# Kernel optimization log

Measured on AMD Instinct MI355X. Metric: run time of the kernel, lower is better.

Reference implementation:

```python
import jax, jax.numpy as jnp
import numpy as np

N, CIN, H, W = 8, 128, 56, 56
COUT, KH, KW = 128, 3, 3
STRIDE, PAD, DIL = 1, 1, 1
HO = (H + 2 * PAD - DIL * (KH - 1) - 1) // STRIDE + 1
WO = (W + 2 * PAD - DIL * (KW - 1) - 1) // STRIDE + 1
K = KH * KW


def setup_inputs() -> dict:
    key = jax.random.key(0)
    k1, k2, k3, k4, k5 = jax.random.split(key, 5)
    x = jax.random.normal(k1, (N, CIN, H, W), dtype=jnp.float32)
    offset = jax.random.normal(k2, (N, 2 * K, HO, WO), dtype=jnp.float32)
    weight = jax.random.normal(k3, (COUT, CIN, KH, KW), dtype=jnp.float32) * (1.0 / np.sqrt(CIN * K))
    bias = jax.random.normal(k4, (COUT,), dtype=jnp.float32) * 0.01
    x2 = jax.random.normal(k5, (N, COUT, HO, WO), dtype=jnp.float32)
    return {"x": x, "offset": offset, "weight": weight, "bias": bias, "x2": x2}


def _deform_conv2d(x, offset, weight, bias):
    n, c, h, w = x.shape
    cout = weight.shape[0]
    # offset layout (torchvision): channels = [dy_0, dx_0, dy_1, dx_1, ...]
    off = offset.reshape(n, K, 2, HO, WO)
    ki = jnp.arange(KH).repeat(KW)          # kernel row index per k   [K]
    kj = jnp.tile(jnp.arange(KW), KH)       # kernel col index per k   [K]
    base_y = (jnp.arange(HO) * STRIDE - PAD)[None, :, None] + (ki * DIL)[:, None, None]  # [K,HO,1]
    base_x = (jnp.arange(WO) * STRIDE - PAD)[None, None, :] + (kj * DIL)[:, None, None]  # [K,1,WO]
    py = base_y[None].astype(x.dtype) + off[:, :, 0]   # [N,K,HO,WO]
    px = base_x[None].astype(x.dtype) + off[:, :, 1]   # [N,K,HO,WO]

    y0 = jnp.floor(py).astype(jnp.int32)
    x0 = jnp.floor(px).astype(jnp.int32)
    wy = py - y0.astype(x.dtype)
    wx = px - x0.astype(x.dtype)

    xf = x.reshape(n, c, h * w)

    def gather(yi, xi):
        valid = (yi >= 0) & (yi < h) & (xi >= 0) & (xi < w)        # [N,K,HO,WO]
        lin = jnp.clip(yi, 0, h - 1) * w + jnp.clip(xi, 0, w - 1)  # [N,K,HO,WO]
        v = jax.vmap(lambda xfn, idx: xfn[:, idx])(xf, lin)        # [N,C,K,HO,WO]
        return v * valid[:, None].astype(x.dtype)

    v00 = gather(y0, x0)
    v01 = gather(y0, x0 + 1)
    v10 = gather(y0 + 1, x0)
    v11 = gather(y0 + 1, x0 + 1)
    wy = wy[:, None]
    wx = wx[:, None]
    cols = (v00 * (1 - wy) * (1 - wx) + v01 * (1 - wy) * wx
            + v10 * wy * (1 - wx) + v11 * wy * wx)                 # [N,C,K,HO,WO]

    wmat = weight.reshape(cout, c, K)
    out = jnp.einsum('nckhw,ock->nohw', cols, wmat)
    return out + bias[None, :, None, None]


def reference(x, offset, weight, bias, x2):
    out = _deform_conv2d(x, offset, weight, bias)
    return jax.nn.relu(out + x2)
```

## Files before the change

### kernel.cpp

```cpp
#include <hip/hip_runtime.h>

#define N_IMG 8
#define CIN   128
#define H_IN  56
#define W_IN  56
#define COUT  128
#define HW    3136
#define TROWS 9
#define TILE_B (TROWS * 56 * 256)
#define PLA_OFF TILE_B
#define PLW_OFF (PLA_OFF + 18432)
#define PLC_OFF (PLW_OFF + 9216)
#define SMEM_TOTAL (PLC_OFF + 4608)

typedef __attribute__((ext_vector_type(8))) short short8;
typedef __attribute__((ext_vector_type(4))) float f32x4;
typedef _Float16 h8 __attribute__((ext_vector_type(8)));

__device__ __forceinline__ unsigned short hb(float f) {
    _Float16 h = (_Float16)f;
    return __builtin_bit_cast(unsigned short, h);
}
__device__ __forceinline__ h8 splat8(unsigned short b) {
    _Float16 s = __builtin_bit_cast(_Float16, b);
    return (h8){s, s, s, s, s, s, s, s};
}
__device__ __forceinline__ void gload16(const void* g, void* l) {
    __builtin_amdgcn_global_load_lds(
        (const __attribute__((address_space(1))) unsigned int*)g,
        (__attribute__((address_space(3))) unsigned int*)l, 16, 0, 0);
}

__global__ __launch_bounds__(256) void prep_kernel(const float* __restrict__ x,
                                                   const float* __restrict__ w,
                                                   unsigned short* __restrict__ xt,
                                                   unsigned short* __restrict__ wr) {
    int b = blockIdx.x;
    int tid = threadIdx.x;
    if (b < 784) {
        int c = tid & 127;
        int half = tid >> 7;
        int n = b / 98;
        int hw0 = (b - n * 98) * 32 + half * 16;
        const float* xp = x + ((size_t)(n * CIN + c)) * HW + hw0;
        unsigned short* op = xt + ((size_t)n * HW + hw0) * CIN + c;
#pragma unroll
        for (int r = 0; r < 16; ++r) op[r * CIN] = hb(xp[r]);
    } else {
        int G = (b - 784) * 256 + tid;
        int lane = G & 63;
        int f = (G >> 6) & 7;
        int kc4 = (G >> 9) & 3;
        int tap = G >> 11;
        int cout = f * 16 + (lane & 15);
        int ch = kc4 * 32 + (lane >> 4) * 8;
        short8 v;
#pragma unroll
        for (int j = 0; j < 8; ++j)
            v[j] = (short)hb(w[((size_t)cout * CIN + ch + j) * 9 + tap]);
        *(short8*)(wr + (size_t)G * 8) = v;
    }
}

__global__ __launch_bounds__(512, 2) void deform_main(
    const float* __restrict__ offset, const float* __restrict__ x2,
    const float* __restrict__ bias, const unsigned short* __restrict__ xt,
    const unsigned short* __restrict__ wr, float* __restrict__ out)
{
    extern __shared__ char smem[];
    int4*  plA = (int4*)(smem + PLA_OFF);
    uint2* plW = (uint2*)(smem + PLW_OFF);
    int*   plC = (int*)(smem + PLC_OFF);

    int tid = threadIdx.x;
    int orig = blockIdx.x;
    int n   = orig & 7;
    int ro0 = (orig >> 3) * 2;

    const char* xim = (const char*)(xt + (size_t)n * HW * CIN);

#pragma unroll
    for (int s = 0; s < 16; ++s) {
        int d = s * 8192 + tid * 16;
        if (d < TILE_B) {
            int p = d >> 8;
            int tr = p / 56;
            int tx = p - tr * 56;
            int gy = min(max(ro0 - 3 + tr, 0), 55);
            int c  = ((d >> 4) & 15) ^ (p & 15);
            gload16(xim + (((gy * 56 + tx) << 8) + (c << 4)), smem + d);
        }
    }

    for (int e = tid; e < 1152; e += 512) {
        int r = (e >= 576) ? 1 : 0;
        int e2 = e - r * 576;
        int tap = e2 >> 6;
        int px  = e2 & 63;
        int wo  = min(px, 55);
        int hor = ro0 + r;
        const float* offp = offset + ((size_t)n * 18 + tap * 2) * HW + hor * 56 + wo;
        float offy = offp[0];
        float offx = offp[HW];
        int ki = tap / 3;
        int kj = tap - ki * 3;
        float py  = (float)(hor - 1 + ki) + offy;
        float pxf = (float)(wo - 1 + kj) + offx;
        float y0f = floorf(py), x0f = floorf(pxf);
        float wy = py - y0f, wx = pxf - x0f;
        int y0 = (int)y0f, x0 = (int)x0f;
        int y1 = y0 + 1, x1 = x0 + 1;
        bool vy0 = (y0 >= 0) && (y0 < H_IN);
        bool vy1 = (y1 >= 0) && (y1 < H_IN);
        bool vx0 = (x0 >= 0) && (x0 < W_IN);
        bool vx1 = (x1 >= 0) && (x1 < W_IN);
        int cy0 = min(max(y0, 0), 55), cy1 = min(max(y1, 0), 55);
        int cx0 = min(max(x0, 0), 55), cx1 = min(max(x1, 0), 55);
        float w00 = (vy0 && vx0) ? (1.f - wy) * (1.f - wx) : 0.f;
        float w01 = (vy0 && vx1) ? (1.f - wy) * wx : 0.f;
        float w10 = (vy1 && vx0) ? wy * (1.f - wx) : 0.f;
        float w11 = (vy1 && vx1) ? wy * wx : 0.f;
        int f0 = (y0 < ro0 - 3 || y0 > ro0 + 5) ? 1 : 0;
        int f1 = (y1 < ro0 - 3 || y1 > ro0 + 5) ? 1 : 0;
        int tr0 = min(max(cy0 + 3 - ro0, 0), TROWS - 1);
        int tr1 = min(max(cy1 + 3 - ro0, 0), TROWS - 1);
        int p00 = tr0 * 56 + cx0, p01 = tr0 * 56 + cx1;
        int p10 = tr1 * 56 + cx0, p11 = tr1 * 56 + cx1;
        int4 A;
        A.x = ((p00 << 8) | ((p00 & 15) << 4)) | ((f0 && w00 != 0.f) ? 0x80000000 : 0);
        A.y = ((p01 << 8) | ((p01 & 15) << 4)) | ((f0 && w01 != 0.f) ? 0x80000000 : 0);
        A.z = ((p10 << 8) | ((p10 & 15) << 4)) | ((f1 && w10 != 0.f) ? 0x80000000 : 0);
        A.w = ((p11 << 8) | ((p11 & 15) << 4)) | ((f1 && w11 != 0.f) ? 0x80000000 : 0);
        plA[e] = A;
        uint2 W;
        W.x = (unsigned)hb(w00) | ((unsigned)hb(w01) << 16);
        W.y = (unsigned)hb(w10) | ((unsigned)hb(w11) << 16);
        plW[e] = W;
        plC[e] = cy0 | (cy1 << 6) | (cx0 << 12) | (cx1 << 18);
    }
    __syncthreads();

    int lane = tid & 63;
    int w8 = tid >> 6;
    int kg = w8 & 1;
    int mt = w8 >> 1;
    int llo = lane & 15, lhi = lane >> 4;
    int slot0 = mt * 32 + llo;
    int slot1 = slot0 + 16;
    int eb0 = (slot0 >> 6) * 576 + (slot0 & 63);
    int eb1 = (slot1 >> 6) * 576 + (slot1 & 63);
    const char* wrb = (const char*)wr;
    int cbs0 = ((kg * 2 + 0) * 4 + lhi) << 4;
    int cbs1 = ((kg * 2 + 1) * 4 + lhi) << 4;

    f32x4 acc[2][8] = {};

    int4  A0 = plA[eb0], A1 = plA[eb1];
    uint2 W0 = plW[eb0], W1 = plW[eb1];

    for (int tap = 0; tap < 9; ++tap) {
        int4 nA0, nA1; uint2 nW0, nW1;
        if (tap < 8) {
            nA0 = plA[eb0 + (tap + 1) * 64]; nW0 = plW[eb0 + (tap + 1) * 64];
            nA1 = plA[eb1 + (tap + 1) * 64]; nW1 = plW[eb1 + (tap + 1) * 64];
        }
        bool fa0 = (unsigned)A0.x >> 31, fa1 = (unsigned)A0.y >> 31;
        bool fa2 = (unsigned)A0.z >> 31, fa3 = (unsigned)A0.w >> 31;
        bool fc0 = (unsigned)A1.x >> 31, fc1 = (unsigned)A1.y >> 31;
        bool fc2 = (unsigned)A1.z >> 31, fc3 = (unsigned)A1.w >> 31;
        bool anyfb = __any(fa0 | fa1 | fa2 | fa3 | fc0 | fc1 | fc2 | fc3);
        int gpa0 = 0, gpa1 = 0, gpa2 = 0, gpa3 = 0;
        int gpc0 = 0, gpc1 = 0, gpc2 = 0, gpc3 = 0;
        if (anyfb) {
            int C0 = plC[eb0 + tap * 64];
            int C1 = plC[eb1 + tap * 64];
            gpa0 = ((C0 & 63) * 56 + ((C0 >> 12) & 63)) << 8;
            gpa1 = ((C0 & 63) * 56 + ((C0 >> 18) & 63)) << 8;
            gpa2 = (((C0 >> 6) & 63) * 56 + ((C0 >> 12) & 63)) << 8;
            gpa3 = (((C0 >> 6) & 63) * 56 + ((C0 >> 18) & 63)) << 8;
            gpc0 = ((C1 & 63) * 56 + ((C1 >> 12) & 63)) << 8;
            gpc1 = ((C1 & 63) * 56 + ((C1 >> 18) & 63)) << 8;
            gpc2 = (((C1 >> 6) & 63) * 56 + ((C1 >> 12) & 63)) << 8;
            gpc3 = (((C1 >> 6) & 63) * 56 + ((C1 >> 18) & 63)) << 8;
        }

#pragma unroll
        for (int kc = 0; kc < 2; ++kc) {
            int cbs = kc ? cbs1 : cbs0;
            const char* bb = wrb + (size_t)((tap * 4 + kg * 2 + kc) * 8) * 1024 + lane * 16;
            h8 bf[8];
#pragma unroll
            for (int f = 0; f < 8; ++f)
                bf[f] = *(const h8*)(bb + f * 1024);

            h8 g0 = *(const h8*)(smem + ((A0.x & 0x7FFFFFFF) ^ cbs));
            h8 g1 = *(const h8*)(smem + ((A0.y & 0x7FFFFFFF) ^ cbs));
            h8 g2 = *(const h8*)(smem + ((A0.z & 0x7FFFFFFF) ^ cbs));
            h8 g3 = *(const h8*)(smem + ((A0.w & 0x7FFFFFFF) ^ cbs));
            if (anyfb) {
                if (fa0) g0 = *(const h8*)(xim + (size_t)(gpa0 + cbs));
                if (fa1) g1 = *(const h8*)(xim + (size_t)(gpa1 + cbs));
                if (fa2) g2 = *(const h8*)(xim + (size_t)(gpa2 + cbs));
                if (fa3) g3 = *(const h8*)(xim + (size_t)(gpa3 + cbs));
            }
            h8 a0 = g0 * splat8((unsigned short)(W0.x & 0xFFFF))
                  + g1 * splat8((unsigned short)(W0.x >> 16))
                  + g2 * splat8((unsigned short)(W0.y & 0xFFFF))
                  + g3 * splat8((unsigned short)(W0.y >> 16));

            h8 h0 = *(const h8*)(smem + ((A1.x & 0x7FFFFFFF) ^ cbs));
            h8 h1 = *(const h8*)(smem + ((A1.y & 0x7FFFFFFF) ^ cbs));
            h8 h2 = *(const h8*)(smem + ((A1.z & 0x7FFFFFFF) ^ cbs));
            h8 h3 = *(const h8*)(smem + ((A1.w & 0x7FFFFFFF) ^ cbs));
            if (anyfb) {
                if (fc0) h0 = *(const h8*)(xim + (size_t)(gpc0 + cbs));
                if (fc1) h1 = *(const h8*)(xim + (size_t)(gpc1 + cbs));
                if (fc2) h2 = *(const h8*)(xim + (size_t)(gpc2 + cbs));
                if (fc3) h3 = *(const h8*)(xim + (size_t)(gpc3 + cbs));
            }
            h8 a1 = h0 * splat8((unsigned short)(W1.x & 0xFFFF))
                  + h1 * splat8((unsigned short)(W1.x >> 16))
                  + h2 * splat8((unsigned short)(W1.y & 0xFFFF))
                  + h3 * splat8((unsigned short)(W1.y >> 16));

#pragma unroll
            for (int f = 0; f < 8; ++f) {
                acc[0][f] = __builtin_amdgcn_mfma_f32_16x16x32_f16(a0, bf[f], acc[0][f], 0, 0, 0);
                acc[1][f] = __builtin_amdgcn_mfma_f32_16x16x32_f16(a1, bf[f], acc[1][f], 0, 0, 0);
            }
        }
        A0 = nA0; A1 = nA1; W0 = nW0; W1 = nW1;
    }

    __syncthreads();
    if (kg == 1) {
#pragma unroll
        for (int q = 0; q < 2; ++q)
#pragma unroll
            for (int f = 0; f < 8; ++f)
                *(f32x4*)(smem + ((((mt * 2 + q) * 8 + f) << 10) + (lane << 4))) = acc[q][f];
    }
    __syncthreads();
    if (kg == 0) {
#pragma unroll
        for (int q = 0; q < 2; ++q)
#pragma unroll
            for (int f = 0; f < 8; ++f) {
                size_t ro = (((mt * 2 + q) * 8 + f) << 10) + (lane << 4);
                acc[q][f] += *(const f32x4*)(smem + ro);
            }

#pragma unroll
        for (int q = 0; q < 2; ++q) {
            int slotq = mt * 32 + q * 16 + lhi * 4;
            int srow = slotq >> 6;
            int wo4 = slotq & 63;
            if (wo4 < 56) {
#pragma unroll
                for (int f = 0; f < 8; ++f) {
                    int cout = f * 16 + llo;
                    float bb = bias[cout];
                    size_t off = ((size_t)(n * COUT + cout)) * HW + (ro0 + srow) * 56 + wo4;
                    f32x4 xv = *(const f32x4*)(x2 + off);
                    f32x4 o;
#pragma unroll
                    for (int r = 0; r < 4; ++r) {
                        float v = acc[q][f][r] + bb + xv[r];
                        o[r] = v > 0.f ? v : 0.f;
                    }
                    *(f32x4*)(out + off) = o;
                }
            }
        }
    }
}

extern "C" void kernel_launch(void* const* d_in, const int* in_sizes, int n_in,
                              void* d_out, int out_size, void* d_ws, size_t ws_size,
                              hipStream_t stream) {
    const float* x      = (const float*)d_in[0];
    const float* offset = (const float*)d_in[1];
    const float* weight = (const float*)d_in[2];
    const float* bias   = (const float*)d_in[3];
    const float* x2     = (const float*)d_in[4];
    float* out = (float*)d_out;

    unsigned short* xt = (unsigned short*)d_ws;
    unsigned short* wr = (unsigned short*)((char*)d_ws + 6422528ULL);

    hipFuncSetAttribute((const void*)deform_main,
                        hipFuncAttributeMaxDynamicSharedMemorySize, SMEM_TOTAL);
    prep_kernel<<<856, 256, 0, stream>>>(x, weight, xt, wr);
    deform_main<<<224, 512, SMEM_TOTAL, stream>>>(offset, x2, bias, xt, wr, out);
}
```

Measured before the change: 32.31 us.

## Software-pipeline LDS gathers one k-chunk ahead of MFMA compute in deform conv

Restructures the tap loop into a double-buffered pipeline. The bilinear corner gathers (LDS reads plus the rare global fallback) for the next k-chunk are issued before the MFMAs of the current chunk, using two register sets. This is meant to hide LDS and global gather latency behind matrix-core work. The cost is higher VGPR pressure, which could lower occupancy or cause spills.

```diff
diff --git a/kernel.cpp b/kernel.cpp
--- a/kernel.cpp
+++ b/kernel.cpp
@@ -30,6 +30,69 @@
         (const __attribute__((address_space(1))) unsigned int*)g,
         (__attribute__((address_space(3))) unsigned int*)l, 16, 0, 0);
 }
+
+#define ISSUE(TAPV, CBS, PA0, PA1, G0,G1,G2,G3,H0,H1,H2,H3)                    \
+  {                                                                            \
+    G0 = *(const h8*)(smem + ((PA0.x & 0x7FFFFFFF) ^ (CBS)));                  \
+    G1 = *(const h8*)(smem + ((PA0.y & 0x7FFFFFFF) ^ (CBS)));                  \
+    G2 = *(const h8*)(smem + ((PA0.z & 0x7FFFFFFF) ^ (CBS)));                  \
+    G3 = *(const h8*)(smem + ((PA0.w & 0x7FFFFFFF) ^ (CBS)));                  \
+    H0 = *(const h8*)(smem + ((PA1.x & 0x7FFFFFFF) ^ (CBS)));                  \
+    H1 = *(const h8*)(smem + ((PA1.y & 0x7FFFFFFF) ^ (CBS)));                  \
+    H2 = *(const h8*)(smem + ((PA1.z & 0x7FFFFFFF) ^ (CBS)));                  \
+    H3 = *(const h8*)(smem + ((PA1.w & 0x7FFFFFFF) ^ (CBS)));                  \
+    bool qa0 = (unsigned)PA0.x >> 31, qa1 = (unsigned)PA0.y >> 31;             \
+    bool qa2 = (unsigned)PA0.z >> 31, qa3 = (unsigned)PA0.w >> 31;             \
+    bool qc0 = (unsigned)PA1.x >> 31, qc1 = (unsigned)PA1.y >> 31;             \
+    bool qc2 = (unsigned)PA1.z >> 31, qc3 = (unsigned)PA1.w >> 31;             \
+    if (__any(qa0 | qa1 | qa2 | qa3 | qc0 | qc1 | qc2 | qc3)) {                \
+      int C0 = plC[eb0 + (TAPV) * 64], C1 = plC[eb1 + (TAPV) * 64];            \
+      if (qa0) G0 = *(const h8*)(xim + (size_t)(int)((((C0 & 63) * 56 + ((C0 >> 12) & 63)) << 8) + (CBS))); \
+      if (qa1) G1 = *(const h8*)(xim + (size_t)(int)((((C0 & 63) * 56 + ((C0 >> 18) & 63)) << 8) + (CBS))); \
+      if (qa2) G2 = *(const h8*)(xim + (size_t)(int)(((((C0 >> 6) & 63) * 56 + ((C0 >> 12) & 63)) << 8) + (CBS))); \
+      if (qa3) G3 = *(const h8*)(xim + (size_t)(int)(((((C0 >> 6) & 63) * 56 + ((C0 >> 18) & 63)) << 8) + (CBS))); \
+      if (qc0) H0 = *(const h8*)(xim + (size_t)(int)((((C1 & 63) * 56 + ((C1 >> 12) & 63)) << 8) + (CBS))); \
+      if (qc1) H1 = *(const h8*)(xim + (size_t)(int)((((C1 & 63) * 56 + ((C1 >> 18) & 63)) << 8) + (CBS))); \
+      if (qc2) H2 = *(const h8*)(xim + (size_t)(int)(((((C1 >> 6) & 63) * 56 + ((C1 >> 12) & 63)) << 8) + (CBS))); \
+      if (qc3) H3 = *(const h8*)(xim + (size_t)(int)(((((C1 >> 6) & 63) * 56 + ((C1 >> 18) & 63)) << 8) + (CBS))); \
+    }                                                                          \
+  }
+
+#define COMPUTE(G0,G1,G2,G3,H0,H1,H2,H3, PW0, PW1, BB)                         \
+  {                                                                            \
+    h8 b0 = *(const h8*)((BB));                                                \
+    h8 b1 = *(const h8*)((BB) + 1024);                                         \
+    h8 b2 = *(const h8*)((BB) + 2048);                                         \
+    h8 b3 = *(const h8*)((BB) + 3072);                                         \
+    h8 b4 = *(const h8*)((BB) + 4096);                                         \
+    h8 b5 = *(const h8*)((BB) + 5120);                                         \
+    h8 b6 = *(const h8*)((BB) + 6144);                                         \
+    h8 b7 = *(const h8*)((BB) + 7168);                                         \
+    h8 a0 = G0 * splat8((unsigned short)(PW0.x & 0xFFFF))                      \
+          + G1 * splat8((unsigned short)(PW0.x >> 16))                         \
+          + G2 * splat8((unsigned short)(PW0.y & 0xFFFF))                      \
+          + G3 * splat8((unsigned short)(PW0.y >> 16));                        \
+    h8 a1 = H0 * splat8((unsigned short)(PW1.x & 0xFFFF))                      \
+          + H1 * splat8((unsigned short)(PW1.x >> 16))                         \
+          + H2 * splat8((unsigned short)(PW1.y & 0xFFFF))                      \
+          + H3 * splat8((unsigned short)(PW1.y >> 16));                        \
+    acc[0][0] = __builtin_amdgcn_mfma_f32_16x16x32_f16(a0, b0, acc[0][0], 0, 0, 0); \
+    acc[1][0] = __builtin_amdgcn_mfma_f32_16x16x32_f16(a1, b0, acc[1][0], 0, 0, 0); \
+    acc[0][1] = __builtin_amdgcn_mfma_f32_16x16x32_f16(a0, b1, acc[0][1], 0, 0, 0); \
+    acc[1][1] = __builtin_amdgcn_mfma_f32_16x16x32_f16(a1, b1, acc[1][1], 0, 0, 0); \
+    acc[0][2] = __builtin_amdgcn_mfma_f32_16x16x32_f16(a0, b2, acc[0][2], 0, 0, 0); \
+    acc[1][2] = __builtin_amdgcn_mfma_f32_16x16x32_f16(a1, b2, acc[1][2], 0, 0, 0); \
+    acc[0][3] = __builtin_amdgcn_mfma_f32_16x16x32_f16(a0, b3, acc[0][3], 0, 0, 0); \
+    acc[1][3] = __builtin_amdgcn_mfma_f32_16x16x32_f16(a1, b3, acc[1][3], 0, 0, 0); \
+    acc[0][4] = __builtin_amdgcn_mfma_f32_16x16x32_f16(a0, b4, acc[0][4], 0, 0, 0); \
+    acc[1][4] = __builtin_amdgcn_mfma_f32_16x16x32_f16(a1, b4, acc[1][4], 0, 0, 0); \
+    acc[0][5] = __builtin_amdgcn_mfma_f32_16x16x32_f16(a0, b5, acc[0][5], 0, 0, 0); \
+    acc[1][5] = __builtin_amdgcn_mfma_f32_16x16x32_f16(a1, b5, acc[1][5], 0, 0, 0); \
+    acc[0][6] = __builtin_amdgcn_mfma_f32_16x16x32_f16(a0, b6, acc[0][6], 0, 0, 0); \
+    acc[1][6] = __builtin_amdgcn_mfma_f32_16x16x32_f16(a1, b6, acc[1][6], 0, 0, 0); \
+    acc[0][7] = __builtin_amdgcn_mfma_f32_16x16x32_f16(a0, b7, acc[0][7], 0, 0, 0); \
+    acc[1][7] = __builtin_amdgcn_mfma_f32_16x16x32_f16(a1, b7, acc[1][7], 0, 0, 0); \
+  }
 
 __global__ __launch_bounds__(256) void prep_kernel(const float* __restrict__ x,
                                                    const float* __restrict__ w,
@@ -158,78 +221,28 @@
     int4  A0 = plA[eb0], A1 = plA[eb1];
     uint2 W0 = plW[eb0], W1 = plW[eb1];
 
-    for (int tap = 0; tap < 9; ++tap) {
+    h8 xa0, xa1, xa2, xa3, ya0, ya1, ya2, ya3;
+    h8 xb0, xb1, xb2, xb3, yb0, yb1, yb2, yb3;
+    ISSUE(0, cbs0, A0, A1, xa0, xa1, xa2, xa3, ya0, ya1, ya2, ya3);
+
+    for (int t = 0; t < 9; ++t) {
         int4 nA0, nA1; uint2 nW0, nW1;
-        if (tap < 8) {
-            nA0 = plA[eb0 + (tap + 1) * 64]; nW0 = plW[eb0 + (tap + 1) * 64];
-            nA1 = plA[eb1 + (tap + 1) * 64]; nW1 = plW[eb1 + (tap + 1) * 64];
-        }
-        bool fa0 = (unsigned)A0.x >> 31, fa1 = (unsigned)A0.y >> 31;
-        bool fa2 = (unsigned)A0.z >> 31, fa3 = (unsigned)A0.w >> 31;
-        bool fc0 = (unsigned)A1.x >> 31, fc1 = (unsigned)A1.y >> 31;
-        bool fc2 = (unsigned)A1.z >> 31, fc3 = (unsigned)A1.w >> 31;
-        bool anyfb = __any(fa0 | fa1 | fa2 | fa3 | fc0 | fc1 | fc2 | fc3);
-        int gpa0 = 0, gpa1 = 0, gpa2 = 0, gpa3 = 0;
-        int gpc0 = 0, gpc1 = 0, gpc2 = 0, gpc3 = 0;
-        if (anyfb) {
-            int C0 = plC[eb0 + tap * 64];
-            int C1 = plC[eb1 + tap * 64];
-            gpa0 = ((C0 & 63) * 56 + ((C0 >> 12) & 63)) << 8;
-            gpa1 = ((C0 & 63) * 56 + ((C0 >> 18) & 63)) << 8;
-            gpa2 = (((C0 >> 6) & 63) * 56 + ((C0 >> 12) & 63)) << 8;
-            gpa3 = (((C0 >> 6) & 63) * 56 + ((C0 >> 18) & 63)) << 8;
-            gpc0 = ((C1 & 63) * 56 + ((C1 >> 12) & 63)) << 8;
-            gpc1 = ((C1 & 63) * 56 + ((C1 >> 18) & 63)) << 8;
-            gpc2 = (((C1 >> 6) & 63) * 56 + ((C1 >> 12) & 63)) << 8;
-            gpc3 = (((C1 >> 6) & 63) * 56 + ((C1 >> 18) & 63)) << 8;
-        }
-
-#pragma unroll
-        for (int kc = 0; kc < 2; ++kc) {
-            int cbs = kc ? cbs1 : cbs0;
-            const char* bb = wrb + (size_t)((tap * 4 + kg * 2 + kc) * 8) * 1024 + lane * 16;
-            h8 bf[8];
-#pragma unroll
-            for (int f = 0; f < 8; ++f)
-                bf[f] = *(const h8*)(bb + f * 1024);
-
-            h8 g0 = *(const h8*)(smem + ((A0.x & 0x7FFFFFFF) ^ cbs));
-            h8 g1 = *(const h8*)(smem + ((A0.y & 0x7FFFFFFF) ^ cbs));
-            h8 g2 = *(const h8*)(smem + ((A0.z & 0x7FFFFFFF) ^ cbs));
-            h8 g3 = *(const h8*)(smem + ((A0.w & 0x7FFFFFFF) ^ cbs));
-            if (anyfb) {
-                if (fa0) g0 = *(const h8*)(xim + (size_t)(gpa0 + cbs));
-                if (fa1) g1 = *(const h8*)(xim + (size_t)(gpa1 + cbs));
-                if (fa2) g2 = *(const h8*)(xim + (size_t)(gpa2 + cbs));
-                if (fa3) g3 = *(const h8*)(xim + (size_t)(gpa3 + cbs));
-            }
-            h8 a0 = g0 * splat8((unsigned short)(W0.x & 0xFFFF))
-                  + g1 * splat8((unsigned short)(W0.x >> 16))
-                  + g2 * splat8((unsigned short)(W0.y & 0xFFFF))
-                  + g3 * splat8((unsigned short)(W0.y >> 16));
-
-            h8 h0 = *(const h8*)(smem + ((A1.x & 0x7FFFFFFF) ^ cbs));
-            h8 h1 = *(const h8*)(smem + ((A1.y & 0x7FFFFFFF) ^ cbs));
-            h8 h2 = *(const h8*)(smem + ((A1.z & 0x7FFFFFFF) ^ cbs));
-            h8 h3 = *(const h8*)(smem + ((A1.w & 0x7FFFFFFF) ^ cbs));
-            if (anyfb) {
-                if (fc0) h0 = *(const h8*)(xim + (size_t)(gpc0 + cbs));
-                if (fc1) h1 = *(const h8*)(xim + (size_t)(gpc1 + cbs));
-                if (fc2) h2 = *(const h8*)(xim + (size_t)(gpc2 + cbs));
-                if (fc3) h3 = *(const h8*)(xim + (size_t)(gpc3 + cbs));
-            }
-            h8 a1 = h0 * splat8((unsigned short)(W1.x & 0xFFFF))
-                  + h1 * splat8((unsigned short)(W1.x >> 16))
-                  + h2 * splat8((unsigned short)(W1.y & 0xFFFF))
-                  + h3 * splat8((unsigned short)(W1.y >> 16));
-
-#pragma unroll
-            for (int f = 0; f < 8; ++f) {
-                acc[0][f] = __builtin_amdgcn_mfma_f32_16x16x32_f16(a0, bf[f], acc[0][f], 0, 0, 0);
-                acc[1][f] = __builtin_amdgcn_mfma_f32_16x16x32_f16(a1, bf[f], acc[1][f], 0, 0, 0);
-            }
-        }
-        A0 = nA0; A1 = nA1; W0 = nW0; W1 = nW1;
+        if (t < 8) {
+            nA0 = plA[eb0 + (t + 1) * 64]; nA1 = plA[eb1 + (t + 1) * 64];
+            nW0 = plW[eb0 + (t + 1) * 64]; nW1 = plW[eb1 + (t + 1) * 64];
+        }
+        ISSUE(t, cbs1, A0, A1, xb0, xb1, xb2, xb3, yb0, yb1, yb2, yb3);
+        {
+            const char* bb = wrb + (size_t)((t * 4 + kg * 2 + 0) * 8) * 1024 + lane * 16;
+            COMPUTE(xa0, xa1, xa2, xa3, ya0, ya1, ya2, ya3, W0, W1, bb);
+        }
+        if (t < 8)
+            ISSUE(t + 1, cbs0, nA0, nA1, xa0, xa1, xa2, xa3, ya0, ya1, ya2, ya3);
+        {
+            const char* bb = wrb + (size_t)((t * 4 + kg * 2 + 1) * 8) * 1024 + lane * 16;
+            COMPUTE(xb0, xb1, xb2, xb3, yb0, yb1, yb2, yb3, W0, W1, bb);
+        }
+        if (t < 8) { A0 = nA0; A1 = nA1; W0 = nW0; W1 = nW1; }
     }
 
     __syncthreads();
```

Result: slower. 37.12 us (+14.9%).

## Route half the sampling slots through global memory gathers instead of LDS

Applied to the files above, without the earlier changes.

Pixel slots whose bit 4 is set now get plain global-image byte offsets in the prepass, with no tile-relative LDS address or fallback flag. In the main loop the second slot group (A1) always gathers from global memory, issued early in each kc iteration, while the first group still reads from LDS with the fallback path. The MFMA loops are split so the a0 products can run while the global loads for a1 are in flight. This is meant to relieve LDS bandwidth pressure by spreading gathers across LDS and L1/L2, at the cost of higher-latency global loads. It also assumes every slot1 (A1) pixel has bit 4 set in the prepass, which depends on the slot-to-pixel mapping and is not visible here.

```diff
diff --git a/kernel.cpp b/kernel.cpp
--- a/kernel.cpp
+++ b/kernel.cpp
@@ -120,17 +120,24 @@
         float w01 = (vy0 && vx1) ? (1.f - wy) * wx : 0.f;
         float w10 = (vy1 && vx0) ? wy * (1.f - wx) : 0.f;
         float w11 = (vy1 && vx1) ? wy * wx : 0.f;
-        int f0 = (y0 < ro0 - 3 || y0 > ro0 + 5) ? 1 : 0;
-        int f1 = (y1 < ro0 - 3 || y1 > ro0 + 5) ? 1 : 0;
-        int tr0 = min(max(cy0 + 3 - ro0, 0), TROWS - 1);
-        int tr1 = min(max(cy1 + 3 - ro0, 0), TROWS - 1);
-        int p00 = tr0 * 56 + cx0, p01 = tr0 * 56 + cx1;
-        int p10 = tr1 * 56 + cx0, p11 = tr1 * 56 + cx1;
         int4 A;
-        A.x = ((p00 << 8) | ((p00 & 15) << 4)) | ((f0 && w00 != 0.f) ? 0x80000000 : 0);
-        A.y = ((p01 << 8) | ((p01 & 15) << 4)) | ((f0 && w01 != 0.f) ? 0x80000000 : 0);
-        A.z = ((p10 << 8) | ((p10 & 15) << 4)) | ((f1 && w10 != 0.f) ? 0x80000000 : 0);
-        A.w = ((p11 << 8) | ((p11 & 15) << 4)) | ((f1 && w11 != 0.f) ? 0x80000000 : 0);
+        if ((px >> 4) & 1) {
+            A.x = (cy0 * 56 + cx0) << 8;
+            A.y = (cy0 * 56 + cx1) << 8;
+            A.z = (cy1 * 56 + cx0) << 8;
+            A.w = (cy1 * 56 + cx1) << 8;
+        } else {
+            int f0 = (y0 < ro0 - 3 || y0 > ro0 + 5) ? 1 : 0;
+            int f1 = (y1 < ro0 - 3 || y1 > ro0 + 5) ? 1 : 0;
+            int tr0 = min(max(cy0 + 3 - ro0, 0), TROWS - 1);
+            int tr1 = min(max(cy1 + 3 - ro0, 0), TROWS - 1);
+            int p00 = tr0 * 56 + cx0, p01 = tr0 * 56 + cx1;
+            int p10 = tr1 * 56 + cx0, p11 = tr1 * 56 + cx1;
+            A.x = ((p00 << 8) | ((p00 & 15) << 4)) | ((f0 && w00 != 0.f) ? 0x80000000 : 0);
+            A.y = ((p01 << 8) | ((p01 & 15) << 4)) | ((f0 && w01 != 0.f) ? 0x80000000 : 0);
+            A.z = ((p10 << 8) | ((p10 & 15) << 4)) | ((f1 && w10 != 0.f) ? 0x80000000 : 0);
+            A.w = ((p11 << 8) | ((p11 & 15) << 4)) | ((f1 && w11 != 0.f) ? 0x80000000 : 0);
+        }
         plA[e] = A;
         uint2 W;
         W.x = (unsigned)hb(w00) | ((unsigned)hb(w01) << 16);
@@ -166,27 +173,23 @@
         }
         bool fa0 = (unsigned)A0.x >> 31, fa1 = (unsigned)A0.y >> 31;
         bool fa2 = (unsigned)A0.z >> 31, fa3 = (unsigned)A0.w >> 31;
-        bool fc0 = (unsigned)A1.x >> 31, fc1 = (unsigned)A1.y >> 31;
-        bool fc2 = (unsigned)A1.z >> 31, fc3 = (unsigned)A1.w >> 31;
-        bool anyfb = __any(fa0 | fa1 | fa2 | fa3 | fc0 | fc1 | fc2 | fc3);
+        bool anyfb = __any(fa0 | fa1 | fa2 | fa3);
         int gpa0 = 0, gpa1 = 0, gpa2 = 0, gpa3 = 0;
-        int gpc0 = 0, gpc1 = 0, gpc2 = 0, gpc3 = 0;
         if (anyfb) {
             int C0 = plC[eb0 + tap * 64];
-            int C1 = plC[eb1 + tap * 64];
             gpa0 = ((C0 & 63) * 56 + ((C0 >> 12) & 63)) << 8;
             gpa1 = ((C0 & 63) * 56 + ((C0 >> 18) & 63)) << 8;
             gpa2 = (((C0 >> 6) & 63) * 56 + ((C0 >> 12) & 63)) << 8;
             gpa3 = (((C0 >> 6) & 63) * 56 + ((C0 >> 18) & 63)) << 8;
-            gpc0 = ((C1 & 63) * 56 + ((C1 >> 12) & 63)) << 8;
-            gpc1 = ((C1 & 63) * 56 + ((C1 >> 18) & 63)) << 8;
-            gpc2 = (((C1 >> 6) & 63) * 56 + ((C1 >> 12) & 63)) << 8;
-            gpc3 = (((C1 >> 6) & 63) * 56 + ((C1 >> 18) & 63)) << 8;
         }
 
 #pragma unroll
         for (int kc = 0; kc < 2; ++kc) {
             int cbs = kc ? cbs1 : cbs0;
+            h8 h0 = *(const h8*)(xim + (size_t)(A1.x + cbs));
+            h8 h1 = *(const h8*)(xim + (size_t)(A1.y + cbs));
+            h8 h2 = *(const h8*)(xim + (size_t)(A1.z + cbs));
+            h8 h3 = *(const h8*)(xim + (size_t)(A1.w + cbs));
             const char* bb = wrb + (size_t)((tap * 4 + kg * 2 + kc) * 8) * 1024 + lane * 16;
             h8 bf[8];
 #pragma unroll
@@ -207,27 +210,17 @@
                   + g1 * splat8((unsigned short)(W0.x >> 16))
                   + g2 * splat8((unsigned short)(W0.y & 0xFFFF))
                   + g3 * splat8((unsigned short)(W0.y >> 16));
-
-            h8 h0 = *(const h8*)(smem + ((A1.x & 0x7FFFFFFF) ^ cbs));
-            h8 h1 = *(const h8*)(smem + ((A1.y & 0x7FFFFFFF) ^ cbs));
-            h8 h2 = *(const h8*)(smem + ((A1.z & 0x7FFFFFFF) ^ cbs));
-            h8 h3 = *(const h8*)(smem + ((A1.w & 0x7FFFFFFF) ^ cbs));
-            if (anyfb) {
-                if (fc0) h0 = *(const h8*)(xim + (size_t)(gpc0 + cbs));
-                if (fc1) h1 = *(const h8*)(xim + (size_t)(gpc1 + cbs));
-                if (fc2) h2 = *(const h8*)(xim + (size_t)(gpc2 + cbs));
-                if (fc3) h3 = *(const h8*)(xim + (size_t)(gpc3 + cbs));
-            }
+#pragma unroll
+            for (int f = 0; f < 8; ++f)
+                acc[0][f] = __builtin_amdgcn_mfma_f32_16x16x32_f16(a0, bf[f], acc[0][f], 0, 0, 0);
+
             h8 a1 = h0 * splat8((unsigned short)(W1.x & 0xFFFF))
                   + h1 * splat8((unsigned short)(W1.x >> 16))
                   + h2 * splat8((unsigned short)(W1.y & 0xFFFF))
                   + h3 * splat8((unsigned short)(W1.y >> 16));
-
-#pragma unroll
-            for (int f = 0; f < 8; ++f) {
-                acc[0][f] = __builtin_amdgcn_mfma_f32_16x16x32_f16(a0, bf[f], acc[0][f], 0, 0, 0);
+#pragma unroll
+            for (int f = 0; f < 8; ++f)
                 acc[1][f] = __builtin_amdgcn_mfma_f32_16x16x32_f16(a1, bf[f], acc[1][f], 0, 0, 0);
-            }
         }
         A0 = nA0; A1 = nA1; W0 = nW0; W1 = nW1;
     }
```

New measurement: 42.07 us. +30.2%, slower.
